# Optimization experiments

Measured on AMD Instinct MI355X. Metric: run time of the kernel, lower is better.

## Reference

```python
import jax, jax.numpy as jnp
import numpy as np

N_TOKENS, D_MODEL, D_FF, N_EXPERTS, TOP_K = 4096, 2048, 1408, 8, 2


def setup_inputs() -> dict:
    key = jax.random.key(0)
    ks = jax.random.split(key, 6)
    s = 0.02
    return {
        "x": jax.random.normal(ks[0], (N_TOKENS, D_MODEL), jnp.float32),
        "topK_indices": jax.random.randint(ks[1], (N_TOKENS, TOP_K), 0, N_EXPERTS, jnp.int32),
        "topK_scores": jax.random.uniform(ks[2], (N_TOKENS, TOP_K), jnp.float32),
        "W_gate": jax.random.normal(ks[3], (N_EXPERTS, D_MODEL, D_FF), jnp.float32) * s,
        "W_up": jax.random.normal(ks[4], (N_EXPERTS, D_MODEL, D_FF), jnp.float32) * s,
        "W_down": jax.random.normal(ks[5], (N_EXPERTS, D_FF, D_MODEL), jnp.float32) * s,
    }


def reference(x, topK_indices, topK_scores, W_gate, W_up, W_down):
    # Combine weights: combine[n, e] = sum over k of score[n, k] where idx[n, k] == e.
    # Mathematically identical to the torch sort/split/index_add dispatch-combine
    # (with multiply_gate_scores=True), expressed densely for a clean jax baseline.
    n = x.shape[0]
    rows = jnp.arange(n)[:, None]  # [N, 1]
    combine = jnp.zeros((n, W_gate.shape[0]), x.dtype).at[rows, topK_indices].add(topK_scores)
    # Per-expert SwiGLU MLP (llama-moe LinearGLUExperts, bias-free).
    h = jax.nn.silu(jnp.einsum("nd,edh->enh", x, W_gate)) * jnp.einsum("nd,edh->enh", x, W_up)
    expert_out = jnp.einsum("enh,ehd->end", h, W_down)  # [E, N, D]
    y = jnp.einsum("ne,end->nd", combine, expert_out)  # weighted scatter-add combine
    return y
```

## Files before the change

kernel.cpp:

```cpp
#include <hip/hip_runtime.h>
#include <hip/hip_bf16.h>


#define NTOK 4096
#define DMODEL 2048
#define DFF 1408
#define NEXP 8
#define TOPK 2
#define NSLOT (NTOK * TOPK)
#define MAX_TILES 160
#define NTILE 72
#define NY1 22
#define NY2 16

typedef short bf16x8 __attribute__((ext_vector_type(8)));
typedef float f32x4 __attribute__((ext_vector_type(4)));

__device__ inline void async16(const void* g, void* l) {
    __builtin_amdgcn_global_load_lds(
        (const __attribute__((address_space(1))) void*)g,
        (__attribute__((address_space(3))) void*)l, 16, 0, 0);
}

__device__ inline int xcd_swz(int bid, int nblk) {
    int q = nblk >> 3, r = nblk & 7;
    int x = bid & 7, p = bid >> 3;
    return (x < r ? x * (q + 1) : r * (q + 1) + (x - r) * q) + p;
}

__global__ __launch_bounds__(256) void route_kernel(
    const int* __restrict__ idx, const float* __restrict__ scores,
    int* __restrict__ meta, int* __restrict__ slot_token, float* __restrict__ slot_score,
    int bm)
{
    __shared__ int counts[NEXP];
    __shared__ int cursor[NEXP];
    int t = threadIdx.x;
    if (t < NEXP) counts[t] = 0;
    __syncthreads();
    for (int i = t; i < NSLOT; i += 256) atomicAdd(&counts[idx[i]], 1);
    __syncthreads();
    if (t == 0) {
        int off = 0, nt = 0;
        for (int e = 0; e < NEXP; e++) {
            cursor[e] = off;
            int c = counts[e];
            for (int s = 0; s < c && nt < MAX_TILES; s += bm) {
                meta[1 + nt * 3 + 0] = e;
                meta[1 + nt * 3 + 1] = off + s;
                meta[1 + nt * 3 + 2] = min(bm, c - s);
                nt++;
            }
            off += c;
        }
        meta[0] = nt;
    }
    __syncthreads();
    for (int i = t; i < NSLOT; i += 256) {
        int e = idx[i];
        int pos = atomicAdd(&cursor[e], 1);
        slot_token[pos] = i / TOPK;
        slot_score[pos] = scores[i];
    }
}

__global__ __launch_bounds__(256) void convert_x(
    const float* __restrict__ x, __hip_bfloat16* __restrict__ xb)
{
    int i = blockIdx.x * 256 + threadIdx.x;
    float4 v = reinterpret_cast<const float4*>(x)[i];
    __hip_bfloat16 o[4] = {(__hip_bfloat16)v.x, (__hip_bfloat16)v.y,
                           (__hip_bfloat16)v.z, (__hip_bfloat16)v.w};
    *reinterpret_cast<uint2*>(&xb[(size_t)i * 4]) = *reinterpret_cast<uint2*>(o);
}

__global__ __launch_bounds__(256) void transpose_convert(
    const float* __restrict__ in, __hip_bfloat16* __restrict__ out, int R, int C)
{
    __shared__ __hip_bfloat16 t[64][72];
    const size_t base = (size_t)blockIdx.z * R * C;
    const int c0 = blockIdx.x * 64, r0 = blockIdx.y * 64;
    const int tid = threadIdx.x;
    const int rl = tid >> 4, c4 = (tid & 15) * 4;
    #pragma unroll
    for (int j = 0; j < 4; j++) {
        int r = rl + j * 16;
        float4 v = *reinterpret_cast<const float4*>(&in[base + (size_t)(r0 + r) * C + c0 + c4]);
        t[c4 + 0][r] = (__hip_bfloat16)v.x;
        t[c4 + 1][r] = (__hip_bfloat16)v.y;
        t[c4 + 2][r] = (__hip_bfloat16)v.z;
        t[c4 + 3][r] = (__hip_bfloat16)v.w;
    }
    __syncthreads();
    const int nl = tid >> 3, k8 = (tid & 7) * 8;
    #pragma unroll
    for (int j = 0; j < 2; j++) {
        int n = nl + j * 32;
        const uint* p = reinterpret_cast<const uint*>(&t[n][k8]);
        uint4 o = {p[0], p[1], p[2], p[3]};
        *reinterpret_cast<uint4*>(&out[base + (size_t)(c0 + n) * R + r0 + k8]) = o;
    }
}

__global__ __launch_bounds__(256, 3) void moe_gemm1_fast(
    const __hip_bfloat16* __restrict__ xb,
    const __hip_bfloat16* __restrict__ WgT, const __hip_bfloat16* __restrict__ WuT,
    const int* __restrict__ meta, const int* __restrict__ slot_token,
    __hip_bfloat16* __restrict__ h)
{
    const int swz = xcd_swz(blockIdx.x, NTILE * NY1);
    const int tile = swz / NY1, yb = swz % NY1;
    if (tile >= meta[0]) return;
    const int e = meta[1 + tile * 3], slot0 = meta[2 + tile * 3], rows = meta[3 + tile * 3];
    const int n0 = yb * 64;

    __shared__ __hip_bfloat16 As[128][64];
    __shared__ __hip_bfloat16 Bgs[64][64];
    __shared__ __hip_bfloat16 Bus[64][64];

    const int tid = threadIdx.x, lane = tid & 63, w = tid >> 6;
    const int wm = w >> 1, wn = w & 1, l15 = lane & 15, lg = lane >> 4;

    uint aoff[4], boff[2];
    #pragma unroll
    for (int i = 0; i < 4; i++) {
        int chunk = tid + i * 256;
        int r = chunk >> 3;
        int slot = slot0 + (r < rows ? r : 0);
        aoff[i] = (uint)(slot_token[slot] * (DMODEL * 2) + (chunk & 7) * 16);
    }
    #pragma unroll
    for (int i = 0; i < 2; i++) {
        int chunk = tid + i * 256;
        int n = chunk >> 3;
        boff[i] = (uint)((n0 + n) * (DMODEL * 2) + (chunk & 7) * 16);
    }
    const char* xbp = (const char*)xb;
    const char* wgp = (const char*)(WgT + (size_t)e * DFF * DMODEL);
    const char* wup = (const char*)(WuT + (size_t)e * DFF * DMODEL);
    char* abase  = (char*)As  + w * 1024;
    char* bgbase = (char*)Bgs + w * 1024;
    char* bubase = (char*)Bus + w * 1024;

    f32x4 ag[4][2] = {};
    f32x4 au[4][2] = {};

    for (int k0 = 0; k0 < DMODEL; k0 += 64) {
        const int kb = k0 * 2;
        #pragma unroll
        for (int i = 0; i < 4; i++) async16(xbp + aoff[i] + kb, abase + i * 4096);
        #pragma unroll
        for (int i = 0; i < 2; i++) {
            async16(wgp + boff[i] + kb, bgbase + i * 4096);
            async16(wup + boff[i] + kb, bubase + i * 4096);
        }
        __syncthreads();
        #pragma unroll
        for (int kk = 0; kk < 2; kk++) {
            bf16x8 a[4], bg[2], bu[2];
            #pragma unroll
            for (int mf = 0; mf < 4; mf++)
                a[mf] = *reinterpret_cast<const bf16x8*>(&As[wm * 64 + mf * 16 + l15][kk * 32 + lg * 8]);
            #pragma unroll
            for (int nf = 0; nf < 2; nf++) {
                bg[nf] = *reinterpret_cast<const bf16x8*>(&Bgs[wn * 32 + nf * 16 + l15][kk * 32 + lg * 8]);
                bu[nf] = *reinterpret_cast<const bf16x8*>(&Bus[wn * 32 + nf * 16 + l15][kk * 32 + lg * 8]);
            }
            #pragma unroll
            for (int mf = 0; mf < 4; mf++)
                #pragma unroll
                for (int nf = 0; nf < 2; nf++) {
                    ag[mf][nf] = __builtin_amdgcn_mfma_f32_16x16x32_bf16(a[mf], bg[nf], ag[mf][nf], 0, 0, 0);
                    au[mf][nf] = __builtin_amdgcn_mfma_f32_16x16x32_bf16(a[mf], bu[nf], au[mf][nf], 0, 0, 0);
                }
        }
        __syncthreads();
    }

    #pragma unroll
    for (int mf = 0; mf < 4; mf++) {
        #pragma unroll
        for (int j = 0; j < 4; j++) {
            int r = wm * 64 + mf * 16 + lg * 4 + j;
            if (r < rows) {
                size_t hrow = (size_t)(slot0 + r) * DFF + n0 + wn * 32;
                #pragma unroll
                for (int nf = 0; nf < 2; nf++) {
                    float g = ag[mf][nf][j], u = au[mf][nf][j];
                    float hv = g / (1.0f + __expf(-g)) * u;
                    h[hrow + nf * 16 + l15] = (__hip_bfloat16)hv;
                }
            }
        }
    }
}

__global__ __launch_bounds__(256, 3) void moe_gemm2_fast(
    const __hip_bfloat16* __restrict__ h, const __hip_bfloat16* __restrict__ WdT,
    const int* __restrict__ meta, const int* __restrict__ slot_token,
    const float* __restrict__ slot_score, float* __restrict__ out)
{
    const int swz = xcd_swz(blockIdx.x, NTILE * NY2);
    const int tile = swz / NY2, yb = swz % NY2;
    if (tile >= meta[0]) return;
    const int e = meta[1 + tile * 3], slot0 = meta[2 + tile * 3], rows = meta[3 + tile * 3];
    const int n0 = yb * 128;

    __shared__ __hip_bfloat16 Ah[128][64];
    __shared__ __hip_bfloat16 Bd[128][64];

    const int tid = threadIdx.x, lane = tid & 63, w = tid >> 6;
    const int wm = w >> 1, wn = w & 1, l15 = lane & 15, lg = lane >> 4;

    uint aoff[4], boff[4];
    #pragma unroll
    for (int i = 0; i < 4; i++) {
        int chunk = tid + i * 256;
        int r = chunk >> 3;
        int slot = slot0 + (r < rows ? r : 0);
        aoff[i] = (uint)(slot * (DFF * 2) + (chunk & 7) * 16);
        boff[i] = (uint)((n0 + r) * (DFF * 2) + (chunk & 7) * 16);
    }
    const char* hp  = (const char*)h;
    const char* wdp = (const char*)(WdT + (size_t)e * DMODEL * DFF);
    char* abase = (char*)Ah + w * 1024;
    char* bbase = (char*)Bd + w * 1024;

    f32x4 acc[4][4] = {};

    for (int k0 = 0; k0 < DFF; k0 += 64) {
        const int kb = k0 * 2;
        #pragma unroll
        for (int i = 0; i < 4; i++) {
            async16(hp  + aoff[i] + kb, abase + i * 4096);
            async16(wdp + boff[i] + kb, bbase + i * 4096);
        }
        __syncthreads();
        #pragma unroll
        for (int kk = 0; kk < 2; kk++) {
            bf16x8 a[4], b[4];
            #pragma unroll
            for (int mf = 0; mf < 4; mf++)
                a[mf] = *reinterpret_cast<const bf16x8*>(&Ah[wm * 64 + mf * 16 + l15][kk * 32 + lg * 8]);
            #pragma unroll
            for (int nf = 0; nf < 4; nf++)
                b[nf] = *reinterpret_cast<const bf16x8*>(&Bd[wn * 64 + nf * 16 + l15][kk * 32 + lg * 8]);
            #pragma unroll
            for (int mf = 0; mf < 4; mf++)
                #pragma unroll
                for (int nf = 0; nf < 4; nf++)
                    acc[mf][nf] = __builtin_amdgcn_mfma_f32_16x16x32_bf16(a[mf], b[nf], acc[mf][nf], 0, 0, 0);
        }
        __syncthreads();
    }

    #pragma unroll
    for (int mf = 0; mf < 4; mf++) {
        #pragma unroll
        for (int j = 0; j < 4; j++) {
            int r = wm * 64 + mf * 16 + lg * 4 + j;
            if (r < rows) {
                int slot = slot0 + r;
                int tok = slot_token[slot];
                float s = slot_score[slot];
                float* orow = out + (size_t)tok * DMODEL + n0 + wn * 64;
                #pragma unroll
                for (int nf = 0; nf < 4; nf++)
                    atomicAdd(&orow[nf * 16 + l15], s * acc[mf][nf][j]);
            }
        }
    }
}

__global__ __launch_bounds__(256) void moe_gemm1(
    const float* __restrict__ x, const float* __restrict__ Wg, const float* __restrict__ Wu,
    const int* __restrict__ meta, const int* __restrict__ slot_token,
    __hip_bfloat16* __restrict__ h)
{
    int tile = blockIdx.x;
    if (tile >= meta[0]) return;
    const int e = meta[1 + tile * 3], slot0 = meta[2 + tile * 3], rows = meta[3 + tile * 3];
    const int n0 = blockIdx.y * 64;
    __shared__ __hip_bfloat16 As[64][72];
    __shared__ __hip_bfloat16 Bgs[64][72];
    __shared__ __hip_bfloat16 Bus[64][72];
    const int tid = threadIdx.x, lane = tid & 63, w = tid >> 6;
    const int wm = w >> 1, wn = w & 1, l15 = lane & 15, lg = lane >> 4;
    const float* __restrict__ WgE = Wg + (size_t)e * DMODEL * DFF;
    const float* __restrict__ WuE = Wu + (size_t)e * DMODEL * DFF;
    f32x4 acc_g[2][2] = {};
    f32x4 acc_u[2][2] = {};
    for (int k0 = 0; k0 < DMODEL; k0 += 64) {
        __syncthreads();
        #pragma unroll
        for (int j = 0; j < 4; j++) {
            int linear = tid + j * 256;
            int r = linear >> 4, c4 = (linear & 15) * 4;
            int tok = (r < rows) ? slot_token[slot0 + r] : 0;
            float4 v = *reinterpret_cast<const float4*>(&x[(size_t)tok * DMODEL + k0 + c4]);
            As[r][c4 + 0] = (__hip_bfloat16)v.x; As[r][c4 + 1] = (__hip_bfloat16)v.y;
            As[r][c4 + 2] = (__hip_bfloat16)v.z; As[r][c4 + 3] = (__hip_bfloat16)v.w;
        }
        #pragma unroll
        for (int j = 0; j < 4; j++) {
            int linear = tid + j * 256;
            int k = linear >> 4, n4 = (linear & 15) * 4;
            float4 vg = *reinterpret_cast<const float4*>(&WgE[(size_t)(k0 + k) * DFF + n0 + n4]);
            Bgs[n4 + 0][k] = (__hip_bfloat16)vg.x; Bgs[n4 + 1][k] = (__hip_bfloat16)vg.y;
            Bgs[n4 + 2][k] = (__hip_bfloat16)vg.z; Bgs[n4 + 3][k] = (__hip_bfloat16)vg.w;
            float4 vu = *reinterpret_cast<const float4*>(&WuE[(size_t)(k0 + k) * DFF + n0 + n4]);
            Bus[n4 + 0][k] = (__hip_bfloat16)vu.x; Bus[n4 + 1][k] = (__hip_bfloat16)vu.y;
            Bus[n4 + 2][k] = (__hip_bfloat16)vu.z; Bus[n4 + 3][k] = (__hip_bfloat16)vu.w;
        }
        __syncthreads();
        #pragma unroll
        for (int kk = 0; kk < 2; kk++) {
            bf16x8 a[2], bg[2], bu[2];
            #pragma unroll
            for (int mf = 0; mf < 2; mf++)
                a[mf] = *reinterpret_cast<const bf16x8*>(&As[wm * 32 + mf * 16 + l15][kk * 32 + lg * 8]);
            #pragma unroll
            for (int nf = 0; nf < 2; nf++) {
                bg[nf] = *reinterpret_cast<const bf16x8*>(&Bgs[wn * 32 + nf * 16 + l15][kk * 32 + lg * 8]);
                bu[nf] = *reinterpret_cast<const bf16x8*>(&Bus[wn * 32 + nf * 16 + l15][kk * 32 + lg * 8]);
            }
            #pragma unroll
            for (int mf = 0; mf < 2; mf++)
                #pragma unroll
                for (int nf = 0; nf < 2; nf++) {
                    acc_g[mf][nf] = __builtin_amdgcn_mfma_f32_16x16x32_bf16(a[mf], bg[nf], acc_g[mf][nf], 0, 0, 0);
                    acc_u[mf][nf] = __builtin_amdgcn_mfma_f32_16x16x32_bf16(a[mf], bu[nf], acc_u[mf][nf], 0, 0, 0);
                }
        }
    }
    #pragma unroll
    for (int mf = 0; mf < 2; mf++)
        #pragma unroll
        for (int nf = 0; nf < 2; nf++)
            #pragma unroll
            for (int j = 0; j < 4; j++) {
                int r = wm * 32 + mf * 16 + lg * 4 + j;
                int c = wn * 32 + nf * 16 + l15;
                if (r < rows) {
                    float g = acc_g[mf][nf][j], u = acc_u[mf][nf][j];
                    h[(size_t)(slot0 + r) * DFF + n0 + c] = (__hip_bfloat16)(g / (1.0f + __expf(-g)) * u);
                }
            }
}

__global__ __launch_bounds__(256) void moe_gemm2(
    const __hip_bfloat16* __restrict__ h, const float* __restrict__ Wd,
    const int* __restrict__ meta, const int* __restrict__ slot_token,
    const float* __restrict__ slot_score, float* __restrict__ out)
{
    int tile = blockIdx.x;
    if (tile >= meta[0]) return;
    const int e = meta[1 + tile * 3], slot0 = meta[2 + tile * 3], rows = meta[3 + tile * 3];
    const int n0 = blockIdx.y * 64;
    __shared__ __hip_bfloat16 As[64][72];
    __shared__ __hip_bfloat16 Bs[64][72];
    const int tid = threadIdx.x, lane = tid & 63, w = tid >> 6;
    const int wm = w >> 1, wn = w & 1, l15 = lane & 15, lg = lane >> 4;
    const float* __restrict__ WdE = Wd + (size_t)e * DFF * DMODEL;
    f32x4 acc[2][2] = {};
    for (int k0 = 0; k0 < DFF; k0 += 64) {
        __syncthreads();
        #pragma unroll
        for (int j = 0; j < 2; j++) {
            int linear = tid + j * 256;
            int r = linear >> 3, c8 = (linear & 7) * 8;
            bf16x8 v = *reinterpret_cast<const bf16x8*>(&h[(size_t)(slot0 + r) * DFF + k0 + c8]);
            *reinterpret_cast<bf16x8*>(&As[r][c8]) = v;
        }
        #pragma unroll
        for (int j = 0; j < 4; j++) {
            int linear = tid + j * 256;
            int k = linear >> 4, n4 = (linear & 15) * 4;
            float4 v = *reinterpret_cast<const float4*>(&WdE[(size_t)(k0 + k) * DMODEL + n0 + n4]);
            Bs[n4 + 0][k] = (__hip_bfloat16)v.x; Bs[n4 + 1][k] = (__hip_bfloat16)v.y;
            Bs[n4 + 2][k] = (__hip_bfloat16)v.z; Bs[n4 + 3][k] = (__hip_bfloat16)v.w;
        }
        __syncthreads();
        #pragma unroll
        for (int kk = 0; kk < 2; kk++) {
            bf16x8 a[2], b[2];
            #pragma unroll
            for (int mf = 0; mf < 2; mf++)
                a[mf] = *reinterpret_cast<const bf16x8*>(&As[wm * 32 + mf * 16 + l15][kk * 32 + lg * 8]);
            #pragma unroll
            for (int nf = 0; nf < 2; nf++)
                b[nf] = *reinterpret_cast<const bf16x8*>(&Bs[wn * 32 + nf * 16 + l15][kk * 32 + lg * 8]);
            #pragma unroll
            for (int mf = 0; mf < 2; mf++)
                #pragma unroll
                for (int nf = 0; nf < 2; nf++)
                    acc[mf][nf] = __builtin_amdgcn_mfma_f32_16x16x32_bf16(a[mf], b[nf], acc[mf][nf], 0, 0, 0);
        }
    }
    #pragma unroll
    for (int mf = 0; mf < 2; mf++)
        #pragma unroll
        for (int nf = 0; nf < 2; nf++)
            #pragma unroll
            for (int j = 0; j < 4; j++) {
                int r = wm * 32 + mf * 16 + lg * 4 + j;
                int c = wn * 32 + nf * 16 + l15;
                if (r < rows) {
                    int slot = slot0 + r;
                    atomicAdd(&out[(size_t)slot_token[slot] * DMODEL + n0 + c],
                              acc[mf][nf][j] * slot_score[slot]);
                }
            }
}

extern "C" void kernel_launch(void* const* d_in, const int* in_sizes, int n_in,
                              void* d_out, int out_size, void* d_ws, size_t ws_size,
                              hipStream_t stream) {
    const float* x      = (const float*)d_in[0];
    const int*   idx    = (const int*)d_in[1];
    const float* scores = (const float*)d_in[2];
    const float* Wg     = (const float*)d_in[3];
    const float* Wu     = (const float*)d_in[4];
    const float* Wd     = (const float*)d_in[5];
    float* out = (float*)d_out;

    char* ws = (char*)d_ws;
    int*   meta       = (int*)ws;
    int*   slot_token = (int*)(ws + 4096);
    float* slot_score = (float*)(ws + 4096 + 34816);

    const size_t XB_OFF = (size_t)1 << 20;
    const size_t HB_OFF = (size_t)20 << 20;
    const size_t WG_OFF = (size_t)44 << 20;
    const size_t WU_OFF = (size_t)92 << 20;
    const size_t WD_OFF = (size_t)140 << 20;
    const size_t NEED   = (size_t)187 << 20;
    const bool fast = ws_size >= NEED;

    hipMemsetAsync(d_out, 0, (size_t)NTOK * DMODEL * sizeof(float), stream);
    route_kernel<<<1, 256, 0, stream>>>(idx, scores, meta, slot_token, slot_score, fast ? 128 : 64);

    if (fast) {
        __hip_bfloat16* xb  = (__hip_bfloat16*)(ws + XB_OFF);
        __hip_bfloat16* hb  = (__hip_bfloat16*)(ws + HB_OFF);
        __hip_bfloat16* WgT = (__hip_bfloat16*)(ws + WG_OFF);
        __hip_bfloat16* WuT = (__hip_bfloat16*)(ws + WU_OFF);
        __hip_bfloat16* WdT = (__hip_bfloat16*)(ws + WD_OFF);

        dim3 td(DMODEL / 64, DFF / 64, NEXP);
        transpose_convert<<<td, 256, 0, stream>>>(Wd, WdT, DFF, DMODEL);
        dim3 tg(DFF / 64, DMODEL / 64, NEXP);
        transpose_convert<<<tg, 256, 0, stream>>>(Wg, WgT, DMODEL, DFF);
        transpose_convert<<<tg, 256, 0, stream>>>(Wu, WuT, DMODEL, DFF);
        convert_x<<<(NTOK * DMODEL / 4) / 256, 256, 0, stream>>>(x, xb);

        moe_gemm1_fast<<<NTILE * NY1, 256, 0, stream>>>(xb, WgT, WuT, meta, slot_token, hb);
        moe_gemm2_fast<<<NTILE * NY2, 256, 0, stream>>>(hb, WdT, meta, slot_token, slot_score, out);
    } else {
        __hip_bfloat16* hb = (__hip_bfloat16*)(ws + 81920);
        dim3 g1(NSLOT / 64 + NEXP, DFF / 64);
        moe_gemm1<<<g1, 256, 0, stream>>>(x, Wg, Wu, meta, slot_token, hb);
        dim3 g2(NSLOT / 64 + NEXP, DMODEL / 64);
        moe_gemm2<<<g2, 256, 0, stream>>>(hb, Wd, meta, slot_token, slot_score, out);
    }
}
```

Measured before the change: 400.6 us.

## Enlarge MoE GEMM tiles to 256 rows with 512 threads and double-buffered LDS

Both fast MoE GEMMs move to 512-thread blocks with 256-row tiles and wider N tiles (128 for gemm1, 256 for gemm2). The route kernel is now told to pad per-expert tiles to 256 rows. Global-to-LDS loads are double-buffered so the next K slice is fetched while the current one is computed. MFMA issue runs under raised priority with intra-iteration barriers, aiming to raise data reuse per block and hide load latency. In exchange it uses more LDS and registers, which may lower occupancy, and the larger tiles waste more work on padded rows at expert boundaries.

```diff
diff --git a/kernel.cpp b/kernel.cpp
--- a/kernel.cpp
+++ b/kernel.cpp
@@ -9,12 +9,14 @@
 #define TOPK 2
 #define NSLOT (NTOK * TOPK)
 #define MAX_TILES 160
-#define NTILE 72
-#define NY1 22
-#define NY2 16
+#define NTILE1 40
+#define NY1 11
+#define NY2 8
 
 typedef short bf16x8 __attribute__((ext_vector_type(8)));
 typedef float f32x4 __attribute__((ext_vector_type(4)));
+
+#define MFMA16(a, b, c) __builtin_amdgcn_mfma_f32_16x16x32_bf16(a, b, c, 0, 0, 0)
 
 __device__ inline void async16(const void* g, void* l) {
     __builtin_amdgcn_global_load_lds(
@@ -102,86 +104,104 @@
     }
 }
 
-__global__ __launch_bounds__(256, 3) void moe_gemm1_fast(
+__global__ __launch_bounds__(512, 2) void moe_gemm1_fast(
     const __hip_bfloat16* __restrict__ xb,
     const __hip_bfloat16* __restrict__ WgT, const __hip_bfloat16* __restrict__ WuT,
     const int* __restrict__ meta, const int* __restrict__ slot_token,
     __hip_bfloat16* __restrict__ h)
 {
-    const int swz = xcd_swz(blockIdx.x, NTILE * NY1);
+    const int swz = xcd_swz(blockIdx.x, NTILE1 * NY1);
     const int tile = swz / NY1, yb = swz % NY1;
     if (tile >= meta[0]) return;
     const int e = meta[1 + tile * 3], slot0 = meta[2 + tile * 3], rows = meta[3 + tile * 3];
-    const int n0 = yb * 64;
-
-    __shared__ __hip_bfloat16 As[128][64];
-    __shared__ __hip_bfloat16 Bgs[64][64];
-    __shared__ __hip_bfloat16 Bus[64][64];
+    const int n0 = yb * 128;
+
+    __shared__ __hip_bfloat16 As[2][256][64];
+    __shared__ __hip_bfloat16 Bgs[2][128][64];
+    __shared__ __hip_bfloat16 Bus[2][128][64];
 
     const int tid = threadIdx.x, lane = tid & 63, w = tid >> 6;
-    const int wm = w >> 1, wn = w & 1, l15 = lane & 15, lg = lane >> 4;
+    const int wm = w >> 2, wn = w & 3, l15 = lane & 15, lg = lane >> 4;
 
     uint aoff[4], boff[2];
     #pragma unroll
     for (int i = 0; i < 4; i++) {
-        int chunk = tid + i * 256;
+        int chunk = tid + i * 512;
         int r = chunk >> 3;
-        int slot = slot0 + (r < rows ? r : 0);
-        aoff[i] = (uint)(slot_token[slot] * (DMODEL * 2) + (chunk & 7) * 16);
+        int rc = r < rows ? r : rows - 1;
+        aoff[i] = (uint)(slot_token[slot0 + rc] * (DMODEL * 2) + (chunk & 7) * 16);
     }
     #pragma unroll
     for (int i = 0; i < 2; i++) {
-        int chunk = tid + i * 256;
+        int chunk = tid + i * 512;
         int n = chunk >> 3;
         boff[i] = (uint)((n0 + n) * (DMODEL * 2) + (chunk & 7) * 16);
     }
     const char* xbp = (const char*)xb;
     const char* wgp = (const char*)(WgT + (size_t)e * DFF * DMODEL);
     const char* wup = (const char*)(WuT + (size_t)e * DFF * DMODEL);
-    char* abase  = (char*)As  + w * 1024;
-    char* bgbase = (char*)Bgs + w * 1024;
-    char* bubase = (char*)Bus + w * 1024;
-
-    f32x4 ag[4][2] = {};
-    f32x4 au[4][2] = {};
-
-    for (int k0 = 0; k0 < DMODEL; k0 += 64) {
-        const int kb = k0 * 2;
-        #pragma unroll
-        for (int i = 0; i < 4; i++) async16(xbp + aoff[i] + kb, abase + i * 4096);
+
+    f32x4 ag[8][2] = {};
+    f32x4 au[8][2] = {};
+
+    auto stage = [&](int kb, int buf) {
+        char* ab = (char*)As[buf]  + w * 1024;
+        char* gb = (char*)Bgs[buf] + w * 1024;
+        char* ub = (char*)Bus[buf] + w * 1024;
+        #pragma unroll
+        for (int i = 0; i < 4; i++) async16(xbp + aoff[i] + kb, ab + i * 8192);
         #pragma unroll
         for (int i = 0; i < 2; i++) {
-            async16(wgp + boff[i] + kb, bgbase + i * 4096);
-            async16(wup + boff[i] + kb, bubase + i * 4096);
+            async16(wgp + boff[i] + kb, gb + i * 8192);
+            async16(wup + boff[i] + kb, ub + i * 8192);
+        }
+    };
+
+    stage(0, 0);
+    __syncthreads();
+
+    for (int kt = 0; kt < DMODEL / 64; ++kt) {
+        const int cur = kt & 1;
+        if (kt + 1 < DMODEL / 64) stage((kt + 1) * 128, cur ^ 1);
+        const __hip_bfloat16 (*Ac)[64]  = As[cur];
+        const __hip_bfloat16 (*Bgc)[64] = Bgs[cur];
+        const __hip_bfloat16 (*Buc)[64] = Bus[cur];
+        #pragma unroll
+        for (int kk = 0; kk < 2; kk++) {
+            bf16x8 bg[2], bu[2];
+            #pragma unroll
+            for (int nf = 0; nf < 2; nf++) {
+                bg[nf] = *(const bf16x8*)&Bgc[wn * 32 + nf * 16 + l15][kk * 32 + lg * 8];
+                bu[nf] = *(const bf16x8*)&Buc[wn * 32 + nf * 16 + l15][kk * 32 + lg * 8];
+            }
+            #pragma unroll
+            for (int mh = 0; mh < 2; mh++) {
+                bf16x8 a[4];
+                #pragma unroll
+                for (int mi = 0; mi < 4; mi++)
+                    a[mi] = *(const bf16x8*)&Ac[wm * 128 + (mh * 4 + mi) * 16 + l15][kk * 32 + lg * 8];
+                __builtin_amdgcn_s_setprio(1);
+                #pragma unroll
+                for (int mi = 0; mi < 4; mi++) {
+                    const int mf = mh * 4 + mi;
+                    #pragma unroll
+                    for (int nf = 0; nf < 2; nf++) {
+                        ag[mf][nf] = MFMA16(a[mi], bg[nf], ag[mf][nf]);
+                        au[mf][nf] = MFMA16(a[mi], bu[nf], au[mf][nf]);
+                    }
+                }
+                __builtin_amdgcn_s_setprio(0);
+                if (!(kk == 1 && mh == 1)) __builtin_amdgcn_s_barrier();
+            }
         }
         __syncthreads();
-        #pragma unroll
-        for (int kk = 0; kk < 2; kk++) {
-            bf16x8 a[4], bg[2], bu[2];
-            #pragma unroll
-            for (int mf = 0; mf < 4; mf++)
-                a[mf] = *reinterpret_cast<const bf16x8*>(&As[wm * 64 + mf * 16 + l15][kk * 32 + lg * 8]);
-            #pragma unroll
-            for (int nf = 0; nf < 2; nf++) {
-                bg[nf] = *reinterpret_cast<const bf16x8*>(&Bgs[wn * 32 + nf * 16 + l15][kk * 32 + lg * 8]);
-                bu[nf] = *reinterpret_cast<const bf16x8*>(&Bus[wn * 32 + nf * 16 + l15][kk * 32 + lg * 8]);
-            }
-            #pragma unroll
-            for (int mf = 0; mf < 4; mf++)
-                #pragma unroll
-                for (int nf = 0; nf < 2; nf++) {
-                    ag[mf][nf] = __builtin_amdgcn_mfma_f32_16x16x32_bf16(a[mf], bg[nf], ag[mf][nf], 0, 0, 0);
-                    au[mf][nf] = __builtin_amdgcn_mfma_f32_16x16x32_bf16(a[mf], bu[nf], au[mf][nf], 0, 0, 0);
-                }
-        }
-        __syncthreads();
-    }
-
-    #pragma unroll
-    for (int mf = 0; mf < 4; mf++) {
+    }
+
+    #pragma unroll
+    for (int mf = 0; mf < 8; mf++) {
         #pragma unroll
         for (int j = 0; j < 4; j++) {
-            int r = wm * 64 + mf * 16 + lg * 4 + j;
+            int r = wm * 128 + mf * 16 + lg * 4 + j;
             if (r < rows) {
                 size_t hrow = (size_t)(slot0 + r) * DFF + n0 + wn * 32;
                 #pragma unroll
@@ -195,70 +215,87 @@
     }
 }
 
-__global__ __launch_bounds__(256, 3) void moe_gemm2_fast(
+__global__ __launch_bounds__(512, 2) void moe_gemm2_fast(
     const __hip_bfloat16* __restrict__ h, const __hip_bfloat16* __restrict__ WdT,
     const int* __restrict__ meta, const int* __restrict__ slot_token,
     const float* __restrict__ slot_score, float* __restrict__ out)
 {
-    const int swz = xcd_swz(blockIdx.x, NTILE * NY2);
+    const int swz = xcd_swz(blockIdx.x, NTILE1 * NY2);
     const int tile = swz / NY2, yb = swz % NY2;
     if (tile >= meta[0]) return;
     const int e = meta[1 + tile * 3], slot0 = meta[2 + tile * 3], rows = meta[3 + tile * 3];
-    const int n0 = yb * 128;
-
-    __shared__ __hip_bfloat16 Ah[128][64];
-    __shared__ __hip_bfloat16 Bd[128][64];
+    const int n0 = yb * 256;
+
+    __shared__ __hip_bfloat16 Ah[2][256][64];
+    __shared__ __hip_bfloat16 Bd[2][256][64];
 
     const int tid = threadIdx.x, lane = tid & 63, w = tid >> 6;
-    const int wm = w >> 1, wn = w & 1, l15 = lane & 15, lg = lane >> 4;
+    const int wm = w >> 2, wn = w & 3, l15 = lane & 15, lg = lane >> 4;
 
     uint aoff[4], boff[4];
     #pragma unroll
     for (int i = 0; i < 4; i++) {
-        int chunk = tid + i * 256;
+        int chunk = tid + i * 512;
         int r = chunk >> 3;
-        int slot = slot0 + (r < rows ? r : 0);
-        aoff[i] = (uint)(slot * (DFF * 2) + (chunk & 7) * 16);
+        int rc = r < rows ? r : rows - 1;
+        aoff[i] = (uint)((slot0 + rc) * (DFF * 2) + (chunk & 7) * 16);
         boff[i] = (uint)((n0 + r) * (DFF * 2) + (chunk & 7) * 16);
     }
     const char* hp  = (const char*)h;
     const char* wdp = (const char*)(WdT + (size_t)e * DMODEL * DFF);
-    char* abase = (char*)Ah + w * 1024;
-    char* bbase = (char*)Bd + w * 1024;
-
-    f32x4 acc[4][4] = {};
-
-    for (int k0 = 0; k0 < DFF; k0 += 64) {
-        const int kb = k0 * 2;
+
+    f32x4 acc[8][4] = {};
+
+    auto stage = [&](int kb, int buf) {
+        char* ab = (char*)Ah[buf] + w * 1024;
+        char* bb = (char*)Bd[buf] + w * 1024;
         #pragma unroll
         for (int i = 0; i < 4; i++) {
-            async16(hp  + aoff[i] + kb, abase + i * 4096);
-            async16(wdp + boff[i] + kb, bbase + i * 4096);
+            async16(hp  + aoff[i] + kb, ab + i * 8192);
+            async16(wdp + boff[i] + kb, bb + i * 8192);
+        }
+    };
+
+    stage(0, 0);
+    __syncthreads();
+
+    for (int kt = 0; kt < DFF / 64; ++kt) {
+        const int cur = kt & 1;
+        if (kt + 1 < DFF / 64) stage((kt + 1) * 128, cur ^ 1);
+        const __hip_bfloat16 (*Ac)[64] = Ah[cur];
+        const __hip_bfloat16 (*Bc)[64] = Bd[cur];
+        #pragma unroll
+        for (int kk = 0; kk < 2; kk++) {
+            bf16x8 b[4];
+            #pragma unroll
+            for (int nf = 0; nf < 4; nf++)
+                b[nf] = *(const bf16x8*)&Bc[wn * 64 + nf * 16 + l15][kk * 32 + lg * 8];
+            #pragma unroll
+            for (int mh = 0; mh < 2; mh++) {
+                bf16x8 a[4];
+                #pragma unroll
+                for (int mi = 0; mi < 4; mi++)
+                    a[mi] = *(const bf16x8*)&Ac[wm * 128 + (mh * 4 + mi) * 16 + l15][kk * 32 + lg * 8];
+                __builtin_amdgcn_s_setprio(1);
+                #pragma unroll
+                for (int mi = 0; mi < 4; mi++) {
+                    const int mf = mh * 4 + mi;
+                    #pragma unroll
+                    for (int nf = 0; nf < 4; nf++)
+                        acc[mf][nf] = MFMA16(a[mi], b[nf], acc[mf][nf]);
+                }
+                __builtin_amdgcn_s_setprio(0);
+                if (!(kk == 1 && mh == 1)) __builtin_amdgcn_s_barrier();
+            }
         }
         __syncthreads();
-        #pragma unroll
-        for (int kk = 0; kk < 2; kk++) {
-            bf16x8 a[4], b[4];
-            #pragma unroll
-            for (int mf = 0; mf < 4; mf++)
-                a[mf] = *reinterpret_cast<const bf16x8*>(&Ah[wm * 64 + mf * 16 + l15][kk * 32 + lg * 8]);
-            #pragma unroll
-            for (int nf = 0; nf < 4; nf++)
-                b[nf] = *reinterpret_cast<const bf16x8*>(&Bd[wn * 64 + nf * 16 + l15][kk * 32 + lg * 8]);
-            #pragma unroll
-            for (int mf = 0; mf < 4; mf++)
-                #pragma unroll
-                for (int nf = 0; nf < 4; nf++)
-                    acc[mf][nf] = __builtin_amdgcn_mfma_f32_16x16x32_bf16(a[mf], b[nf], acc[mf][nf], 0, 0, 0);
-        }
-        __syncthreads();
-    }
-
-    #pragma unroll
-    for (int mf = 0; mf < 4; mf++) {
+    }
+
+    #pragma unroll
+    for (int mf = 0; mf < 8; mf++) {
         #pragma unroll
         for (int j = 0; j < 4; j++) {
-            int r = wm * 64 + mf * 16 + lg * 4 + j;
+            int r = wm * 128 + mf * 16 + lg * 4 + j;
             if (r < rows) {
                 int slot = slot0 + r;
                 int tok = slot_token[slot];
@@ -328,8 +365,8 @@
             for (int mf = 0; mf < 2; mf++)
                 #pragma unroll
                 for (int nf = 0; nf < 2; nf++) {
-                    acc_g[mf][nf] = __builtin_amdgcn_mfma_f32_16x16x32_bf16(a[mf], bg[nf], acc_g[mf][nf], 0, 0, 0);
-                    acc_u[mf][nf] = __builtin_amdgcn_mfma_f32_16x16x32_bf16(a[mf], bu[nf], acc_u[mf][nf], 0, 0, 0);
+                    acc_g[mf][nf] = MFMA16(a[mf], bg[nf], acc_g[mf][nf]);
+                    acc_u[mf][nf] = MFMA16(a[mf], bu[nf], acc_u[mf][nf]);
                 }
         }
     }
@@ -394,7 +431,7 @@
             for (int mf = 0; mf < 2; mf++)
                 #pragma unroll
                 for (int nf = 0; nf < 2; nf++)
-                    acc[mf][nf] = __builtin_amdgcn_mfma_f32_16x16x32_bf16(a[mf], b[nf], acc[mf][nf], 0, 0, 0);
+                    acc[mf][nf] = MFMA16(a[mf], b[nf], acc[mf][nf]);
         }
     }
     #pragma unroll
@@ -438,7 +475,7 @@
     const bool fast = ws_size >= NEED;
 
     hipMemsetAsync(d_out, 0, (size_t)NTOK * DMODEL * sizeof(float), stream);
-    route_kernel<<<1, 256, 0, stream>>>(idx, scores, meta, slot_token, slot_score, fast ? 128 : 64);
+    route_kernel<<<1, 256, 0, stream>>>(idx, scores, meta, slot_token, slot_score, fast ? 256 : 64);
 
     if (fast) {
         __hip_bfloat16* xb  = (__hip_bfloat16*)(ws + XB_OFF);
@@ -454,8 +491,8 @@
         transpose_convert<<<tg, 256, 0, stream>>>(Wu, WuT, DMODEL, DFF);
         convert_x<<<(NTOK * DMODEL / 4) / 256, 256, 0, stream>>>(x, xb);
 
-        moe_gemm1_fast<<<NTILE * NY1, 256, 0, stream>>>(xb, WgT, WuT, meta, slot_token, hb);
-        moe_gemm2_fast<<<NTILE * NY2, 256, 0, stream>>>(hb, WdT, meta, slot_token, slot_score, out);
+        moe_gemm1_fast<<<NTILE1 * NY1, 512, 0, stream>>>(xb, WgT, WuT, meta, slot_token, hb);
+        moe_gemm2_fast<<<NTILE1 * NY2, 512, 0, stream>>>(hb, WdT, meta, slot_token, slot_score, out);
     } else {
         __hip_bfloat16* hb = (__hip_bfloat16*)(ws + 81920);
         dim3 g1(NSLOT / 64 + NEXP, DFF / 64);
```

Result: slower. 463.8 us (+15.8%).

## Double-buffer LDS tiles with async prefetch and XOR-swizzle in MoE GEMMs

Applied to the files above, without the earlier changes.

Both fast grouped GEMM kernels now keep two LDS stages and issue async global-to-LDS loads two K-tiles ahead, so memory latency overlaps the MFMA work instead of waiting on a barrier every iteration. LDS columns are XOR-swizzled to cut bank conflicts on the fragment reads. MFMAs are wrapped in raised wave priority. The doubled LDS footprint lowers the occupancy hint from 3 to 2 blocks per CU, trading latency hiding across waves for explicit pipelining.

```diff
diff --git a/kernel.cpp b/kernel.cpp
--- a/kernel.cpp
+++ b/kernel.cpp
@@ -15,6 +15,8 @@
 
 typedef short bf16x8 __attribute__((ext_vector_type(8)));
 typedef float f32x4 __attribute__((ext_vector_type(4)));
+
+#define MFMA16(a, b, c) __builtin_amdgcn_mfma_f32_16x16x32_bf16(a, b, c, 0, 0, 0)
 
 __device__ inline void async16(const void* g, void* l) {
     __builtin_amdgcn_global_load_lds(
@@ -102,7 +104,7 @@
     }
 }
 
-__global__ __launch_bounds__(256, 3) void moe_gemm1_fast(
+__global__ __launch_bounds__(256, 2) void moe_gemm1_fast(
     const __hip_bfloat16* __restrict__ xb,
     const __hip_bfloat16* __restrict__ WgT, const __hip_bfloat16* __restrict__ WuT,
     const int* __restrict__ meta, const int* __restrict__ slot_token,
@@ -114,67 +116,89 @@
     const int e = meta[1 + tile * 3], slot0 = meta[2 + tile * 3], rows = meta[3 + tile * 3];
     const int n0 = yb * 64;
 
-    __shared__ __hip_bfloat16 As[128][64];
-    __shared__ __hip_bfloat16 Bgs[64][64];
-    __shared__ __hip_bfloat16 Bus[64][64];
+    __shared__ __hip_bfloat16 As[2][128][64];
+    __shared__ __hip_bfloat16 Bgs[2][64][64];
+    __shared__ __hip_bfloat16 Bus[2][64][64];
 
     const int tid = threadIdx.x, lane = tid & 63, w = tid >> 6;
     const int wm = w >> 1, wn = w & 1, l15 = lane & 15, lg = lane >> 4;
+    const int swb = l15 & 7;
 
     uint aoff[4], boff[2];
     #pragma unroll
     for (int i = 0; i < 4; i++) {
         int chunk = tid + i * 256;
         int r = chunk >> 3;
-        int slot = slot0 + (r < rows ? r : 0);
-        aoff[i] = (uint)(slot_token[slot] * (DMODEL * 2) + (chunk & 7) * 16);
+        int rc = r < rows ? r : rows - 1;
+        int slot8 = (chunk & 7) ^ ((chunk >> 3) & 7);
+        aoff[i] = (uint)(slot_token[slot0 + rc] * (DMODEL * 2) + slot8 * 16);
     }
     #pragma unroll
     for (int i = 0; i < 2; i++) {
         int chunk = tid + i * 256;
         int n = chunk >> 3;
-        boff[i] = (uint)((n0 + n) * (DMODEL * 2) + (chunk & 7) * 16);
+        int slot8 = (chunk & 7) ^ ((chunk >> 3) & 7);
+        boff[i] = (uint)((n0 + n) * (DMODEL * 2) + slot8 * 16);
     }
     const char* xbp = (const char*)xb;
     const char* wgp = (const char*)(WgT + (size_t)e * DFF * DMODEL);
     const char* wup = (const char*)(WuT + (size_t)e * DFF * DMODEL);
-    char* abase  = (char*)As  + w * 1024;
-    char* bgbase = (char*)Bgs + w * 1024;
-    char* bubase = (char*)Bus + w * 1024;
 
     f32x4 ag[4][2] = {};
     f32x4 au[4][2] = {};
 
-    for (int k0 = 0; k0 < DMODEL; k0 += 64) {
-        const int kb = k0 * 2;
-        #pragma unroll
-        for (int i = 0; i < 4; i++) async16(xbp + aoff[i] + kb, abase + i * 4096);
+    auto stage = [&](int kt, int buf) {
+        const int kb = kt * 128;
+        char* ab = (char*)As[buf]  + w * 1024;
+        char* gb = (char*)Bgs[buf] + w * 1024;
+        char* ub = (char*)Bus[buf] + w * 1024;
+        #pragma unroll
+        for (int i = 0; i < 4; i++) async16(xbp + aoff[i] + kb, ab + i * 4096);
         #pragma unroll
         for (int i = 0; i < 2; i++) {
-            async16(wgp + boff[i] + kb, bgbase + i * 4096);
-            async16(wup + boff[i] + kb, bubase + i * 4096);
-        }
-        __syncthreads();
+            async16(wgp + boff[i] + kb, gb + i * 4096);
+            async16(wup + boff[i] + kb, ub + i * 4096);
+        }
+    };
+
+    constexpr int NT = DMODEL / 64;
+    stage(0, 0);
+    stage(1, 1);
+
+    for (int kt = 0; kt < NT; ++kt) {
+        const int cur = kt & 1;
+        if (kt < NT - 1) asm volatile("s_waitcnt vmcnt(8)" ::: "memory");
+        else             asm volatile("s_waitcnt vmcnt(0)" ::: "memory");
+        __builtin_amdgcn_s_barrier();
+
+        bf16x8 a[2][4], bg[2][2], bu[2][2];
         #pragma unroll
         for (int kk = 0; kk < 2; kk++) {
-            bf16x8 a[4], bg[2], bu[2];
+            const int cb = ((kk * 4 + lg) ^ swb) * 16;
             #pragma unroll
             for (int mf = 0; mf < 4; mf++)
-                a[mf] = *reinterpret_cast<const bf16x8*>(&As[wm * 64 + mf * 16 + l15][kk * 32 + lg * 8]);
+                a[kk][mf] = *(const bf16x8*)((const char*)&As[cur][wm * 64 + mf * 16 + l15][0] + cb);
             #pragma unroll
             for (int nf = 0; nf < 2; nf++) {
-                bg[nf] = *reinterpret_cast<const bf16x8*>(&Bgs[wn * 32 + nf * 16 + l15][kk * 32 + lg * 8]);
-                bu[nf] = *reinterpret_cast<const bf16x8*>(&Bus[wn * 32 + nf * 16 + l15][kk * 32 + lg * 8]);
-            }
+                bg[kk][nf] = *(const bf16x8*)((const char*)&Bgs[cur][wn * 32 + nf * 16 + l15][0] + cb);
+                bu[kk][nf] = *(const bf16x8*)((const char*)&Bus[cur][wn * 32 + nf * 16 + l15][0] + cb);
+            }
+        }
+        asm volatile("s_waitcnt lgkmcnt(0)" ::: "memory");
+        __builtin_amdgcn_s_barrier();
+        if (kt + 2 < NT) stage(kt + 2, cur);
+
+        __builtin_amdgcn_s_setprio(1);
+        #pragma unroll
+        for (int kk = 0; kk < 2; kk++)
             #pragma unroll
             for (int mf = 0; mf < 4; mf++)
                 #pragma unroll
                 for (int nf = 0; nf < 2; nf++) {
-                    ag[mf][nf] = __builtin_amdgcn_mfma_f32_16x16x32_bf16(a[mf], bg[nf], ag[mf][nf], 0, 0, 0);
-                    au[mf][nf] = __builtin_amdgcn_mfma_f32_16x16x32_bf16(a[mf], bu[nf], au[mf][nf], 0, 0, 0);
+                    ag[mf][nf] = MFMA16(a[kk][mf], bg[kk][nf], ag[mf][nf]);
+                    au[mf][nf] = MFMA16(a[kk][mf], bu[kk][nf], au[mf][nf]);
                 }
-        }
-        __syncthreads();
+        __builtin_amdgcn_s_setprio(0);
     }
 
     #pragma unroll
@@ -195,7 +219,7 @@
     }
 }
 
-__global__ __launch_bounds__(256, 3) void moe_gemm2_fast(
+__global__ __launch_bounds__(256, 2) void moe_gemm2_fast(
     const __hip_bfloat16* __restrict__ h, const __hip_bfloat16* __restrict__ WdT,
     const int* __restrict__ meta, const int* __restrict__ slot_token,
     const float* __restrict__ slot_score, float* __restrict__ out)
@@ -206,52 +230,73 @@
     const int e = meta[1 + tile * 3], slot0 = meta[2 + tile * 3], rows = meta[3 + tile * 3];
     const int n0 = yb * 128;
 
-    __shared__ __hip_bfloat16 Ah[128][64];
-    __shared__ __hip_bfloat16 Bd[128][64];
+    __shared__ __hip_bfloat16 Ah[2][128][64];
+    __shared__ __hip_bfloat16 Bd[2][128][64];
 
     const int tid = threadIdx.x, lane = tid & 63, w = tid >> 6;
     const int wm = w >> 1, wn = w & 1, l15 = lane & 15, lg = lane >> 4;
+    const int swb = l15 & 7;
 
     uint aoff[4], boff[4];
     #pragma unroll
     for (int i = 0; i < 4; i++) {
         int chunk = tid + i * 256;
         int r = chunk >> 3;
-        int slot = slot0 + (r < rows ? r : 0);
-        aoff[i] = (uint)(slot * (DFF * 2) + (chunk & 7) * 16);
-        boff[i] = (uint)((n0 + r) * (DFF * 2) + (chunk & 7) * 16);
+        int rc = r < rows ? r : rows - 1;
+        int slot8 = (chunk & 7) ^ ((chunk >> 3) & 7);
+        aoff[i] = (uint)((slot0 + rc) * (DFF * 2) + slot8 * 16);
+        boff[i] = (uint)((n0 + r) * (DFF * 2) + slot8 * 16);
     }
     const char* hp  = (const char*)h;
     const char* wdp = (const char*)(WdT + (size_t)e * DMODEL * DFF);
-    char* abase = (char*)Ah + w * 1024;
-    char* bbase = (char*)Bd + w * 1024;
 
     f32x4 acc[4][4] = {};
 
-    for (int k0 = 0; k0 < DFF; k0 += 64) {
-        const int kb = k0 * 2;
+    auto stage = [&](int kt, int buf) {
+        const int kb = kt * 128;
+        char* ab = (char*)Ah[buf] + w * 1024;
+        char* bb = (char*)Bd[buf] + w * 1024;
         #pragma unroll
         for (int i = 0; i < 4; i++) {
-            async16(hp  + aoff[i] + kb, abase + i * 4096);
-            async16(wdp + boff[i] + kb, bbase + i * 4096);
-        }
-        __syncthreads();
+            async16(hp  + aoff[i] + kb, ab + i * 4096);
+            async16(wdp + boff[i] + kb, bb + i * 4096);
+        }
+    };
+
+    constexpr int NT = DFF / 64;
+    stage(0, 0);
+    stage(1, 1);
+
+    for (int kt = 0; kt < NT; ++kt) {
+        const int cur = kt & 1;
+        if (kt < NT - 1) asm volatile("s_waitcnt vmcnt(8)" ::: "memory");
+        else             asm volatile("s_waitcnt vmcnt(0)" ::: "memory");
+        __builtin_amdgcn_s_barrier();
+
+        bf16x8 a[2][4], b[2][4];
         #pragma unroll
         for (int kk = 0; kk < 2; kk++) {
-            bf16x8 a[4], b[4];
+            const int cb = ((kk * 4 + lg) ^ swb) * 16;
             #pragma unroll
             for (int mf = 0; mf < 4; mf++)
-                a[mf] = *reinterpret_cast<const bf16x8*>(&Ah[wm * 64 + mf * 16 + l15][kk * 32 + lg * 8]);
+                a[kk][mf] = *(const bf16x8*)((const char*)&Ah[cur][wm * 64 + mf * 16 + l15][0] + cb);
             #pragma unroll
             for (int nf = 0; nf < 4; nf++)
-                b[nf] = *reinterpret_cast<const bf16x8*>(&Bd[wn * 64 + nf * 16 + l15][kk * 32 + lg * 8]);
+                b[kk][nf] = *(const bf16x8*)((const char*)&Bd[cur][wn * 64 + nf * 16 + l15][0] + cb);
+        }
+        asm volatile("s_waitcnt lgkmcnt(0)" ::: "memory");
+        __builtin_amdgcn_s_barrier();
+        if (kt + 2 < NT) stage(kt + 2, cur);
+
+        __builtin_amdgcn_s_setprio(1);
+        #pragma unroll
+        for (int kk = 0; kk < 2; kk++)
             #pragma unroll
             for (int mf = 0; mf < 4; mf++)
                 #pragma unroll
                 for (int nf = 0; nf < 4; nf++)
-                    acc[mf][nf] = __builtin_amdgcn_mfma_f32_16x16x32_bf16(a[mf], b[nf], acc[mf][nf], 0, 0, 0);
-        }
-        __syncthreads();
+                    acc[mf][nf] = MFMA16(a[kk][mf], b[kk][nf], acc[mf][nf]);
+        __builtin_amdgcn_s_setprio(0);
     }
 
     #pragma unroll
@@ -328,8 +373,8 @@
             for (int mf = 0; mf < 2; mf++)
                 #pragma unroll
                 for (int nf = 0; nf < 2; nf++) {
-                    acc_g[mf][nf] = __builtin_amdgcn_mfma_f32_16x16x32_bf16(a[mf], bg[nf], acc_g[mf][nf], 0, 0, 0);
-                    acc_u[mf][nf] = __builtin_amdgcn_mfma_f32_16x16x32_bf16(a[mf], bu[nf], acc_u[mf][nf], 0, 0, 0);
+                    acc_g[mf][nf] = MFMA16(a[mf], bg[nf], acc_g[mf][nf]);
+                    acc_u[mf][nf] = MFMA16(a[mf], bu[nf], acc_u[mf][nf]);
                 }
         }
     }
@@ -394,7 +439,7 @@
             for (int mf = 0; mf < 2; mf++)
                 #pragma unroll
                 for (int nf = 0; nf < 2; nf++)
-                    acc[mf][nf] = __builtin_amdgcn_mfma_f32_16x16x32_bf16(a[mf], b[nf], acc[mf][nf], 0, 0, 0);
+                    acc[mf][nf] = MFMA16(a[mf], b[nf], acc[mf][nf]);
         }
     }
     #pragma unroll
```

Result: faster. 361.4 us (-9.8%).
